# Kernel optimization log

Measured on AMD Instinct MI355X. Metric: run time of the kernel, lower is better.

## Reference

```python
import jax, jax.numpy as jnp
import numpy as np

D_MODEL = 2048
NUM_Q_HEADS = 32
NUM_KV_HEADS = 8
HEAD_DIM = D_MODEL // NUM_Q_HEADS  # 64
NUM_GROUPS = NUM_Q_HEADS // NUM_KV_HEADS  # 4


def setup_inputs() -> dict:
    key = jax.random.key(0)
    ks = jax.random.split(key, 9)
    s = 1.0 / np.sqrt(D_MODEL)
    x = jax.random.normal(ks[0], (2, 2048, D_MODEL), dtype=jnp.float32)
    Wq = jax.random.uniform(ks[1], (D_MODEL, NUM_Q_HEADS * HEAD_DIM), jnp.float32, -s, s)
    bq = jax.random.uniform(ks[2], (NUM_Q_HEADS * HEAD_DIM,), jnp.float32, -s, s)
    Wk = jax.random.uniform(ks[3], (D_MODEL, NUM_KV_HEADS * HEAD_DIM), jnp.float32, -s, s)
    bk = jax.random.uniform(ks[4], (NUM_KV_HEADS * HEAD_DIM,), jnp.float32, -s, s)
    Wv = jax.random.uniform(ks[5], (D_MODEL, NUM_KV_HEADS * HEAD_DIM), jnp.float32, -s, s)
    bv = jax.random.uniform(ks[6], (NUM_KV_HEADS * HEAD_DIM,), jnp.float32, -s, s)
    Wo = jax.random.uniform(ks[7], (D_MODEL, D_MODEL), jnp.float32, -s, s)
    bo = jax.random.uniform(ks[8], (D_MODEL,), jnp.float32, -s, s)
    return {"x": x, "Wq": Wq, "bq": bq, "Wk": Wk, "bk": bk,
            "Wv": Wv, "bv": bv, "Wo": Wo, "bo": bo}


def reference(x, Wq, bq, Wk, bk, Wv, bv, Wo, bo):
    B, T, C = x.shape
    Hkv, G, Dh = NUM_KV_HEADS, NUM_GROUPS, HEAD_DIM
    # projections
    q = (x @ Wq + bq).reshape(B, T, Hkv, G, Dh)   # group G query heads per kv head
    k = (x @ Wk + bk).reshape(B, T, Hkv, Dh)
    v = (x @ Wv + bv).reshape(B, T, Hkv, Dh)
    scale = 1.0 / np.sqrt(Dh).astype(np.float32)
    # scores: [B, Hkv, G, T, T] (kv head broadcast over its G query heads)
    scores = jnp.einsum('btkgd,bskd->bkgts', q, k) * scale
    attn = jax.nn.softmax(scores, axis=-1)
    out = jnp.einsum('bkgts,bskd->btkgd', attn, v).reshape(B, T, C)
    return out @ Wo + bo
```

## Files before the change

### kernel.cpp

```cpp
#include <hip/hip_runtime.h>
#include <cstdint>
#include <cstddef>
#include <math.h>

typedef uint16_t bf16;
typedef __attribute__((ext_vector_type(8))) __bf16 bf16x8;
typedef __attribute__((ext_vector_type(2))) float f32x2;
typedef __attribute__((ext_vector_type(4))) float f32x4;
typedef __attribute__((ext_vector_type(16))) float f32x16;

#define MFMA16(a,b,c) __builtin_amdgcn_mfma_f32_16x16x32_bf16((a),(b),(c),0,0,0)
#define MFMA32(a,b,c) __builtin_amdgcn_mfma_f32_32x32x16_bf16((a),(b),(c),0,0,0)

__device__ __forceinline__ uint16_t f2bf(float f){
  uint32_t u = __float_as_uint(f);
  return (uint16_t)((u + 0x7fffu + ((u >> 16) & 1u)) >> 16);
}
__device__ __forceinline__ uint32_t pk2(float lo, float hi){
  return (uint32_t)f2bf(lo) | ((uint32_t)f2bf(hi) << 16);
}

__device__ __forceinline__ void gload_lds16(const void* g, void* l){
  __builtin_amdgcn_global_load_lds((const __attribute__((address_space(1))) void*)g,
                                   (__attribute__((address_space(3))) void*)l, 16, 0, 0);
}

__global__ void k_convert(const float* __restrict__ in, bf16* __restrict__ out, int n){
  int i = (blockIdx.x * 256 + threadIdx.x) * 4;
  if (i >= n) return;
  float4 v = *reinterpret_cast<const float4*>(in + i);
  uint32_t lo = pk2(v.x, v.y);
  uint32_t hi = pk2(v.z, v.w);
  uint2 pkv = make_uint2(lo, hi);
  *reinterpret_cast<uint2*>(out + i) = pkv;
}

__global__ void k_transposeW(const float* __restrict__ in, bf16* __restrict__ out, int R, int C){
  __shared__ float tile[64][65];
  int c0 = blockIdx.x * 64, r0 = blockIdx.y * 64;
  int t = threadIdx.x;
  int fx = t & 15, fy = t >> 4;
  #pragma unroll
  for (int i = 0; i < 4; i++){
    int r = fy + i*16;
    float4 v = *reinterpret_cast<const float4*>(in + (size_t)(r0 + r)*C + c0 + fx*4);
    tile[r][fx*4+0] = v.x; tile[r][fx*4+1] = v.y;
    tile[r][fx*4+2] = v.z; tile[r][fx*4+3] = v.w;
  }
  __syncthreads();
  int gx = t & 7, gy = t >> 3;
  #pragma unroll
  for (int i = 0; i < 2; i++){
    int c = gy + i*32;
    int rr = gx*8;
    union { bf16 h[8]; uint4 u; } pk_;
    #pragma unroll
    for (int j = 0; j < 8; j++) pk_.h[j] = f2bf(tile[rr+j][c]);
    *reinterpret_cast<uint4*>(out + (size_t)(c0 + c)*R + r0 + rr) = pk_.u;
  }
}

__device__ __forceinline__ void gemm128_core(
    const bf16* __restrict__ Abase, const bf16* __restrict__ Btbase,
    int lda, int ldb, int K, bf16* As, bf16* Bs, f32x4 acc[4][4])
{
  const int tid = threadIdx.x;
  const int wid = tid >> 6, lane = tid & 63;
  const int wr = wid >> 1, wc = wid & 1;
  const int lr = lane & 15, lg = lane >> 4;
  const f32x4 vzero = {0.f, 0.f, 0.f, 0.f};

  #pragma unroll
  for (int m = 0; m < 4; m++)
    #pragma unroll
    for (int n = 0; n < 4; n++)
      acc[m][n] = vzero;

  int srcA[4], srcB[4], dOff[4];
  #pragma unroll
  for (int i = 0; i < 4; i++){
    int d = i*4096 + wid*1024 + lane*16;
    int row = d >> 7, sp = (d >> 4) & 7;
    int sl = sp ^ (row & 7);
    srcA[i] = row * lda + sl * 8;
    srcB[i] = row * ldb + sl * 8;
    dOff[i] = i*4096 + wid*1024;
  }

  for (int k0 = 0; k0 < K; k0 += 64){
    #pragma unroll
    for (int i = 0; i < 4; i++)
      gload_lds16(Abase + k0 + srcA[i], (char*)As + dOff[i]);
    #pragma unroll
    for (int i = 0; i < 4; i++)
      gload_lds16(Btbase + k0 + srcB[i], (char*)Bs + dOff[i]);
    __syncthreads();
    #pragma unroll
    for (int ks = 0; ks < 2; ks++){
      bf16x8 af[4], bfr[4];
      #pragma unroll
      for (int m = 0; m < 4; m++){
        int row = wr*64 + m*16 + lr;
        int sp = (ks*4 + lg) ^ (row & 7);
        af[m] = *reinterpret_cast<const bf16x8*>(As + row*64 + sp*8);
      }
      #pragma unroll
      for (int n = 0; n < 4; n++){
        int row = wc*64 + n*16 + lr;
        int sp = (ks*4 + lg) ^ (row & 7);
        bfr[n] = *reinterpret_cast<const bf16x8*>(Bs + row*64 + sp*8);
      }
      #pragma unroll
      for (int m = 0; m < 4; m++)
        #pragma unroll
        for (int n = 0; n < 4; n++)
          acc[m][n] = MFMA16(af[m], bfr[n], acc[m][n]);
    }
    __syncthreads();
  }
}

__device__ __forceinline__ void gemm256_core(
    const bf16* __restrict__ Abase, const bf16* __restrict__ Btbase,
    char* lds, f32x4 acc[8][4])
{
  const int tid = threadIdx.x;
  const int wid = tid >> 6, lane = tid & 63;
  const int wm = wid >> 2, wn = wid & 3;
  const int lr = lane & 15, lg = lane >> 4;
  const f32x4 vzero = {0.f, 0.f, 0.f, 0.f};
  #pragma unroll
  for (int m = 0; m < 8; m++)
    #pragma unroll
    for (int n = 0; n < 4; n++)
      acc[m][n] = vzero;

  int srcH[2];
  #pragma unroll
  for (int i = 0; i < 2; i++){
    int db = i*8192 + tid*16;
    int row = db >> 7, sp = (db >> 4) & 7, sl = sp ^ (row & 7);
    srcH[i] = row*2048 + sl*8;
  }
  const int dOf = wid*1024;

  int ksl[2];
  #pragma unroll
  for (int ks = 0; ks < 2; ks++) ksl[ks] = (((ks*4 + lg) ^ (lr & 7)) << 4);
  const int aB = wm*16384 + lr*128;
  const int bB = 32768 + (wn >> 1)*16384 + (wn & 1)*8192 + lr*128;

  const bf16* Ab1 = Abase + 128*2048;
  const bf16* Bb1 = Btbase + 128*2048;

  #define STG_HALF(dstOff, gsrc) do { \
    gload_lds16((gsrc) + srcH[0], lds + (dstOff) + dOf); \
    gload_lds16((gsrc) + srcH[1], lds + (dstOff) + 8192 + dOf); \
  } while(0)

  STG_HALF(0,     Abase);
  STG_HALF(16384, Ab1);
  STG_HALF(32768, Btbase);
  STG_HALF(49152, Bb1);
  STG_HALF(65536, Abase + 64);
  asm volatile("s_waitcnt vmcnt(2)" ::: "memory");
  __builtin_amdgcn_s_barrier();

  bf16x8 afr[4][2], bfr[4][2];
  for (int t = 0; t < 32; t++){
    const int bo = (t & 1) * 65536;
    const int nb = bo ^ 65536;

    #pragma unroll
    for (int am = 0; am < 4; am++)
      #pragma unroll
      for (int ks = 0; ks < 2; ks++)
        afr[am][ks] = *reinterpret_cast<const bf16x8*>(lds + bo + aB + am*2048 + ksl[ks]);
    #pragma unroll
    for (int bn = 0; bn < 2; bn++)
      #pragma unroll
      for (int ks = 0; ks < 2; ks++)
        bfr[bn][ks] = *reinterpret_cast<const bf16x8*>(lds + bo + bB + bn*2048 + ksl[ks]);
    if (t < 31) STG_HALF(nb + 16384, Ab1 + (t+1)*64);
    __builtin_amdgcn_s_barrier();
    asm volatile("s_waitcnt lgkmcnt(0)" ::: "memory");
    __builtin_amdgcn_sched_barrier(0);
    __builtin_amdgcn_s_setprio(1);
    #pragma unroll
    for (int am = 0; am < 4; am++)
      #pragma unroll
      for (int bn = 0; bn < 2; bn++)
        #pragma unroll
        for (int ks = 0; ks < 2; ks++)
          acc[am][bn] = MFMA16(afr[am][ks], bfr[bn][ks], acc[am][bn]);
    __builtin_amdgcn_s_setprio(0);
    __builtin_amdgcn_s_barrier();

    #pragma unroll
    for (int bn = 2; bn < 4; bn++)
      #pragma unroll
      for (int ks = 0; ks < 2; ks++)
        bfr[bn][ks] = *reinterpret_cast<const bf16x8*>(lds + bo + bB + bn*2048 + ksl[ks]);
    if (t < 31) STG_HALF(nb + 32768, Btbase + (t+1)*64);
    __builtin_amdgcn_s_barrier();
    asm volatile("s_waitcnt lgkmcnt(0)" ::: "memory");
    __builtin_amdgcn_sched_barrier(0);
    __builtin_amdgcn_s_setprio(1);
    #pragma unroll
    for (int am = 0; am < 4; am++)
      #pragma unroll
      for (int bn = 2; bn < 4; bn++)
        #pragma unroll
        for (int ks = 0; ks < 2; ks++)
          acc[am][bn] = MFMA16(afr[am][ks], bfr[bn][ks], acc[am][bn]);
    __builtin_amdgcn_s_setprio(0);
    __builtin_amdgcn_s_barrier();

    #pragma unroll
    for (int am = 0; am < 4; am++)
      #pragma unroll
      for (int ks = 0; ks < 2; ks++)
        afr[am][ks] = *reinterpret_cast<const bf16x8*>(lds + bo + aB + (am+4)*2048 + ksl[ks]);
    if (t < 31) STG_HALF(nb + 49152, Bb1 + (t+1)*64);
    __builtin_amdgcn_s_barrier();
    asm volatile("s_waitcnt lgkmcnt(0)" ::: "memory");
    __builtin_amdgcn_sched_barrier(0);
    __builtin_amdgcn_s_setprio(1);
    #pragma unroll
    for (int am = 0; am < 4; am++)
      #pragma unroll
      for (int bn = 0; bn < 2; bn++)
        #pragma unroll
        for (int ks = 0; ks < 2; ks++)
          acc[am+4][bn] = MFMA16(afr[am][ks], bfr[bn][ks], acc[am+4][bn]);
    __builtin_amdgcn_s_setprio(0);
    __builtin_amdgcn_s_barrier();

    if (t < 30) STG_HALF(bo, Abase + (t+2)*64);
    __builtin_amdgcn_s_barrier();
    __builtin_amdgcn_s_setprio(1);
    #pragma unroll
    for (int am = 0; am < 4; am++)
      #pragma unroll
      for (int bn = 2; bn < 4; bn++)
        #pragma unroll
        for (int ks = 0; ks < 2; ks++)
          acc[am+4][bn] = MFMA16(afr[am][ks], bfr[bn][ks], acc[am+4][bn]);
    __builtin_amdgcn_s_setprio(0);
    if (t < 30)      asm volatile("s_waitcnt vmcnt(2)" ::: "memory");
    else if (t == 30) asm volatile("s_waitcnt vmcnt(0)" ::: "memory");
    __builtin_amdgcn_sched_barrier(0);
    __builtin_amdgcn_s_barrier();
  }
  #undef STG_HALF
}

__global__ __launch_bounds__(512, 1) void k_qkv(
    const bf16* __restrict__ xb,
    const bf16* __restrict__ WqT, const bf16* __restrict__ WkT, const bf16* __restrict__ WvT,
    const float* __restrict__ bq, const float* __restrict__ bk, const float* __restrict__ bv,
    bf16* __restrict__ qo, bf16* __restrict__ ko, bf16* __restrict__ vtp)
{
  __shared__ __align__(16) char lds[131072];
  int by = blockIdx.y;
  const bf16* Bt; const float* bias; int mode; int y; float scale = 1.f;
  if (by < 8){       y = by;    Bt = WqT + (size_t)y*256*2048; bias = bq + y*256; mode = 0; scale = 0.18033688011112042f; }
  else if (by < 10){ y = by-8;  Bt = WkT + (size_t)y*256*2048; bias = bk + y*256; mode = 1; }
  else {             y = by-10; Bt = WvT + (size_t)y*256*2048; bias = bv + y*256; mode = 2; }
  int m0 = blockIdx.x * 256;
  f32x4 acc[8][4];
  gemm256_core(xb + (size_t)m0*2048, Bt, lds, acc);
  const int tid = threadIdx.x, wid = tid >> 6, lane = tid & 63;
  const int wm = wid >> 2, wn = wid & 3, lr = lane & 15, lg = lane >> 4;
  if (mode == 2){
    #pragma unroll
    for (int bn = 0; bn < 4; bn++){
      int c = wn*64 + bn*16 + lr;
      float bb = bias[c];
      int CL = y*256 + c;
      #pragma unroll
      for (int am = 0; am < 8; am++){
        int row0 = m0 + wm*128 + am*16 + lg*4;
        int bi = row0 >> 11, tl = row0 & 2047;
        union { bf16 h[4]; uint2 u; } pk_;
        #pragma unroll
        for (int r = 0; r < 4; r++) pk_.h[r] = f2bf(acc[am][bn][r] + bb);
        *reinterpret_cast<uint2*>(vtp + ((size_t)bi*512 + CL)*2048 + tl) = pk_.u;
      }
    }
  } else {
    bf16* outp = (mode == 0) ? (qo + y*256) : (ko + y*256);
    int ldc = (mode == 0) ? 2048 : 512;
    #pragma unroll
    for (int bn = 0; bn < 4; bn++){
      int c = wn*64 + bn*16 + lr;
      float bb = bias[c];
      #pragma unroll
      for (int am = 0; am < 8; am++)
        #pragma unroll
        for (int r = 0; r < 4; r++){
          int row = m0 + wm*128 + am*16 + lg*4 + r;
          outp[(size_t)row*ldc + c] = f2bf((acc[am][bn][r] + bb) * scale);
        }
    }
  }
}

__global__ __launch_bounds__(256, 2) void k_oproj(
    const bf16* __restrict__ ab, const bf16* __restrict__ WoT,
    const float* __restrict__ bo, float* __restrict__ outp)
{
  __shared__ __align__(16) bf16 As[128*64];
  __shared__ __align__(16) bf16 Bs[128*64];
  int m0 = blockIdx.x * 128, n0 = blockIdx.y * 128;
  f32x4 acc[4][4];
  gemm128_core(ab + (size_t)m0*2048, WoT + (size_t)n0*2048, 2048, 2048, 2048, As, Bs, acc);
  const int tid = threadIdx.x, wid = tid >> 6, lane = tid & 63;
  const int wr = wid >> 1, wc = wid & 1, lr = lane & 15, lg = lane >> 4;
  #pragma unroll
  for (int n = 0; n < 4; n++){
    int col = n0 + wc*64 + n*16 + lr;
    float bb = bo[col];
    #pragma unroll
    for (int m = 0; m < 4; m++)
      #pragma unroll
      for (int r = 0; r < 4; r++){
        int row = m0 + wr*64 + m*16 + lg*4 + r;
        outp[(size_t)row*2048 + col] = acc[m][n][r] + bb;
      }
  }
}

__global__ __launch_bounds__(512, 2) void k_flash(
    const bf16* __restrict__ q, const bf16* __restrict__ kmat,
    const bf16* __restrict__ vt, bf16* __restrict__ ao)
{
  __shared__ __align__(16) char lds[98304];
  const int tid = threadIdx.x;
  const int wid = tid >> 6, lane = tid & 63;
  const int l31 = lane & 31, hi = lane >> 5;
  const int bh = blockIdx.y;
  const int b = bh >> 5, hq = bh & 31, kvh = hq >> 2;
  const int qt = blockIdx.x;
  const int qrow0 = b*2048 + qt*512 + wid*64;

  bf16x8 qf[2][4];
  #pragma unroll
  for (int g = 0; g < 2; g++){
    const bf16* qrow = q + (size_t)(qrow0 + g*32 + l31)*2048 + hq*64 + hi*8;
    #pragma unroll
    for (int t = 0; t < 4; t++)
      qf[g][t] = *reinterpret_cast<const bf16x8*>(qrow + t*16);
  }

  f32x16 oacc[2][2];
  #pragma unroll
  for (int g = 0; g < 2; g++)
    #pragma unroll
    for (int n = 0; n < 2; n++)
      #pragma unroll
      for (int r = 0; r < 16; r++) oacc[g][n][r] = 0.f;
  float rsg[2][2];
  rsg[0][0]=0.f; rsg[0][1]=0.f; rsg[1][0]=0.f; rsg[1][1]=0.f;
  const f32x16 zv = {0.f,0.f,0.f,0.f,0.f,0.f,0.f,0.f,0.f,0.f,0.f,0.f,0.f,0.f,0.f,0.f};

  const int r7 = l31 & 7;
  int A[4];
  #pragma unroll
  for (int j = 0; j < 4; j++)
    A[j] = l31*128 + (((2*j + hi) ^ r7) << 4);

  const bf16* kbase = kmat + (size_t)b*2048*512 + kvh*64;
  const bf16* vbase = vt + ((size_t)b*512 + kvh*64)*2048;

  int kSrc[2], vSrc[2];
  const int dOf = wid*1024;
  #pragma unroll
  for (int i = 0; i < 2; i++){
    int kdb = i*8192 + tid*16;
    int krow = kdb >> 7, ksp = (kdb >> 4) & 7, ksl = ksp ^ (krow & 7);
    kSrc[i] = krow*512 + ksl*8;
    int o = tid*16;
    int vrow = o >> 7, vsp = (o >> 4) & 7, vsl = vsp ^ (vrow & 7);
    vSrc[i] = vrow*2048 + i*64 + vsl*8;
  }

  #define STAGE(bo, st_) do { \
    const bf16* kb_ = kbase + (size_t)(st_)*128*512; \
    const bf16* vb_ = vbase + (st_)*128; \
    gload_lds16(kb_ + kSrc[0], lds + (bo) + dOf); \
    gload_lds16(kb_ + kSrc[1], lds + (bo) + 8192 + dOf); \
    gload_lds16(vb_ + vSrc[0], lds + 49152 + (bo) + dOf); \
    gload_lds16(vb_ + vSrc[1], lds + 49152 + (bo) + 8192 + dOf); \
  } while(0)

  #define LDK(j, imm) (*reinterpret_cast<const bf16x8*>(lds + kOff + A[j] + (imm)))
  #define LDV(j, imm) (*reinterpret_cast<const bf16x8*>(lds + 49152 + kOff + A[j] + (imm)))

  STAGE(0, 0);
  STAGE(16384, 1);

  int kOff = 0;
  int sOff = 32768;
  for (int st = 0; st < 16; st++){
    if (st == 15) asm volatile("s_waitcnt vmcnt(0)" ::: "memory");
    else          asm volatile("s_waitcnt vmcnt(4)" ::: "memory");
    __builtin_amdgcn_sched_barrier(0);
    __builtin_amdgcn_s_barrier();
    __builtin_amdgcn_sched_barrier(0);
    if (st < 14){
      STAGE(sOff, st+2);
      sOff = (sOff == 32768) ? 0 : sOff + 16384;
    }

    #pragma unroll
    for (int c = 0; c < 2; c++){
      f32x16 sc[2][2];
      __builtin_amdgcn_s_setprio(1);
      #pragma unroll
      for (int t = 0; t < 4; t++){
        bf16x8 af0 = LDK(t, c*8192);
        bf16x8 af1 = LDK(t, c*8192 + 4096);
        if (t == 0){
          sc[0][0] = MFMA32(af0, qf[0][0], zv);
          sc[1][0] = MFMA32(af0, qf[1][0], zv);
          sc[0][1] = MFMA32(af1, qf[0][0], zv);
          sc[1][1] = MFMA32(af1, qf[1][0], zv);
        } else {
          sc[0][0] = MFMA32(af0, qf[0][t], sc[0][0]);
          sc[1][0] = MFMA32(af0, qf[1][t], sc[1][0]);
          sc[0][1] = MFMA32(af1, qf[0][t], sc[0][1]);
          sc[1][1] = MFMA32(af1, qf[1][t], sc[1][1]);
        }
      }
      __builtin_amdgcn_s_setprio(0);

      uint32_t pw[2][2][8];
      #pragma unroll
      for (int g = 0; g < 2; g++){
        #pragma unroll
        for (int n = 0; n < 2; n++)
          #pragma unroll
          for (int j = 0; j < 8; j++){
            float plo = __builtin_amdgcn_exp2f(sc[g][n][2*j]);
            float phi = __builtin_amdgcn_exp2f(sc[g][n][2*j+1]);
            rsg[g][j & 1] += plo + phi;
            asm("v_cvt_pk_bf16_f32 %0, %1, %2" : "=v"(pw[g][n][j]) : "v"(plo), "v"(phi));
          }
        #pragma unroll
        for (int n = 0; n < 2; n++)
          #pragma unroll
          for (int h = 0; h < 2; h++){
            asm volatile("v_permlane32_swap_b32 %0, %1" : "+v"(pw[g][n][h*4+0]), "+v"(pw[g][n][h*4+2]));
            asm volatile("v_permlane32_swap_b32 %0, %1" : "+v"(pw[g][n][h*4+1]), "+v"(pw[g][n][h*4+3]));
          }
      }

      __builtin_amdgcn_s_setprio(1);
      #pragma unroll
      for (int kk = 0; kk < 4; kk++){
        int n = kk >> 1, h = kk & 1;
        union { uint32_t w[4]; bf16x8 v; } pa0, pa1;
        #pragma unroll
        for (int w_ = 0; w_ < 4; w_++){ pa0.w[w_] = pw[0][n][h*4+w_]; pa1.w[w_] = pw[1][n][h*4+w_]; }
        #pragma unroll
        for (int nd = 0; nd < 2; nd++){
          bf16x8 vf = LDV(kk, c*8192 + nd*4096);
          oacc[0][nd] = MFMA32(pa0.v, vf, oacc[0][nd]);
          oacc[1][nd] = MFMA32(pa1.v, vf, oacc[1][nd]);
        }
      }
      __builtin_amdgcn_s_setprio(0);
    }
    kOff = (kOff == 32768) ? 0 : kOff + 16384;
  }
  #undef STAGE
  #undef LDK
  #undef LDV

  #pragma unroll
  for (int g = 0; g < 2; g++){
    float rs = rsg[g][0] + rsg[g][1];
    float l = rs + __shfl_xor(rs, 32);
    float linv = 1.f / l;
    float lv[16];
    #pragma unroll
    for (int r = 0; r < 16; r++){
      int qi = (r & 3) + 8*(r >> 2) + 4*hi;
      lv[r] = __shfl(linv, qi);
    }
    #pragma unroll
    for (int nd = 0; nd < 2; nd++)
      #pragma unroll
      for (int r = 0; r < 16; r++){
        int qi = (r & 3) + 8*(r >> 2) + 4*hi;
        int row = qrow0 + g*32 + qi;
        ao[(size_t)row*2048 + hq*64 + nd*32 + l31] = f2bf(oacc[g][nd][r] * lv[r]);
      }
  }
}

extern "C" void kernel_launch(void* const* d_in, const int* in_sizes, int n_in,
                              void* d_out, int out_size, void* d_ws, size_t ws_size,
                              hipStream_t stream)
{
  const float* x  = (const float*)d_in[0];
  const float* Wq = (const float*)d_in[1];
  const float* bq = (const float*)d_in[2];
  const float* Wk = (const float*)d_in[3];
  const float* bk = (const float*)d_in[4];
  const float* Wv = (const float*)d_in[5];
  const float* bv = (const float*)d_in[6];
  const float* Wo = (const float*)d_in[7];
  const float* bo = (const float*)d_in[8];
  float* out = (float*)d_out;

  char* ws = (char*)d_ws;
  size_t off = 0;
  auto alloc = [&](size_t bytes){ char* p = ws + off; off += (bytes + 255) & ~(size_t)255; return p; };
  bf16* xb  = (bf16*)alloc(2*2048*2048*2);
  bf16* WqT = (bf16*)alloc(2048*2048*2);
  bf16* WkT = (bf16*)alloc(512*2048*2);
  bf16* WvT = (bf16*)alloc(512*2048*2);
  bf16* WoT = (bf16*)alloc(2048*2048*2);
  bf16* qb  = (bf16*)alloc(4096*2048*2);
  bf16* kb  = (bf16*)alloc((size_t)4096*512*2);
  bf16* vtb = (bf16*)alloc((size_t)4096*512*2);
  bf16* aob = xb;

  k_convert<<<8192, 256, 0, stream>>>(x, xb, 2*2048*2048);
  k_transposeW<<<dim3(32,32), 256, 0, stream>>>(Wq, WqT, 2048, 2048);
  k_transposeW<<<dim3(8,32),  256, 0, stream>>>(Wk, WkT, 2048, 512);
  k_transposeW<<<dim3(8,32),  256, 0, stream>>>(Wv, WvT, 2048, 512);
  k_transposeW<<<dim3(32,32), 256, 0, stream>>>(Wo, WoT, 2048, 2048);
  k_qkv<<<dim3(16,12), 512, 0, stream>>>(xb, WqT, WkT, WvT, bq, bk, bv, qb, kb, vtb);
  k_flash<<<dim3(4,64), 512, 0, stream>>>(qb, kb, vtb, aob);
  k_oproj<<<dim3(32,16), 256, 0, stream>>>(aob, WoT, bo, out);
}
```

Before: 194.3 us.

## Replace output projection GEMM with pipelined 256x128 tile kernel

The output projection previously used a simple 128x128 tile GEMM that loaded A and B into LDS, synchronized, computed, and synchronized again, with no overlap. It now uses a 512-thread 256x128 tile core with a triple-buffered A stage and double-buffered B stage. Global-to-LDS loads for later k-steps are issued while MFMAs run, with explicit waitcnt, barrier and priority control. The grid drops from 512 to 256 blocks at one block per CU, which reduces redundant B reads and hides load latency, but risks lower occupancy and tail imbalance.

```diff
diff --git a/kernel.cpp b/kernel.cpp
--- a/kernel.cpp
+++ b/kernel.cpp
@@ -57,66 +57,6 @@
     #pragma unroll
     for (int j = 0; j < 8; j++) pk_.h[j] = f2bf(tile[rr+j][c]);
     *reinterpret_cast<uint4*>(out + (size_t)(c0 + c)*R + r0 + rr) = pk_.u;
-  }
-}
-
-__device__ __forceinline__ void gemm128_core(
-    const bf16* __restrict__ Abase, const bf16* __restrict__ Btbase,
-    int lda, int ldb, int K, bf16* As, bf16* Bs, f32x4 acc[4][4])
-{
-  const int tid = threadIdx.x;
-  const int wid = tid >> 6, lane = tid & 63;
-  const int wr = wid >> 1, wc = wid & 1;
-  const int lr = lane & 15, lg = lane >> 4;
-  const f32x4 vzero = {0.f, 0.f, 0.f, 0.f};
-
-  #pragma unroll
-  for (int m = 0; m < 4; m++)
-    #pragma unroll
-    for (int n = 0; n < 4; n++)
-      acc[m][n] = vzero;
-
-  int srcA[4], srcB[4], dOff[4];
-  #pragma unroll
-  for (int i = 0; i < 4; i++){
-    int d = i*4096 + wid*1024 + lane*16;
-    int row = d >> 7, sp = (d >> 4) & 7;
-    int sl = sp ^ (row & 7);
-    srcA[i] = row * lda + sl * 8;
-    srcB[i] = row * ldb + sl * 8;
-    dOff[i] = i*4096 + wid*1024;
-  }
-
-  for (int k0 = 0; k0 < K; k0 += 64){
-    #pragma unroll
-    for (int i = 0; i < 4; i++)
-      gload_lds16(Abase + k0 + srcA[i], (char*)As + dOff[i]);
-    #pragma unroll
-    for (int i = 0; i < 4; i++)
-      gload_lds16(Btbase + k0 + srcB[i], (char*)Bs + dOff[i]);
-    __syncthreads();
-    #pragma unroll
-    for (int ks = 0; ks < 2; ks++){
-      bf16x8 af[4], bfr[4];
-      #pragma unroll
-      for (int m = 0; m < 4; m++){
-        int row = wr*64 + m*16 + lr;
-        int sp = (ks*4 + lg) ^ (row & 7);
-        af[m] = *reinterpret_cast<const bf16x8*>(As + row*64 + sp*8);
-      }
-      #pragma unroll
-      for (int n = 0; n < 4; n++){
-        int row = wc*64 + n*16 + lr;
-        int sp = (ks*4 + lg) ^ (row & 7);
-        bfr[n] = *reinterpret_cast<const bf16x8*>(Bs + row*64 + sp*8);
-      }
-      #pragma unroll
-      for (int m = 0; m < 4; m++)
-        #pragma unroll
-        for (int n = 0; n < 4; n++)
-          acc[m][n] = MFMA16(af[m], bfr[n], acc[m][n]);
-    }
-    __syncthreads();
   }
 }
 
@@ -253,6 +193,107 @@
     __builtin_amdgcn_s_barrier();
   }
   #undef STG_HALF
+}
+
+__device__ __forceinline__ void gemm256x128_core(
+    const bf16* __restrict__ Abase, const bf16* __restrict__ Btbase,
+    char* lds, f32x4 acc[2][8])
+{
+  const int tid = threadIdx.x;
+  const int wid = tid >> 6, lane = tid & 63;
+  const int lr = lane & 15, lg = lane >> 4;
+  const f32x4 vzero = {0.f, 0.f, 0.f, 0.f};
+  #pragma unroll
+  for (int m = 0; m < 2; m++)
+    #pragma unroll
+    for (int n = 0; n < 8; n++)
+      acc[m][n] = vzero;
+
+  int srcH[2];
+  #pragma unroll
+  for (int i = 0; i < 2; i++){
+    int db = i*8192 + tid*16;
+    int row = db >> 7, sp = (db >> 4) & 7, sl = sp ^ (row & 7);
+    srcH[i] = row*2048 + sl*8;
+  }
+  const int dOf = wid*1024;
+
+  int ksl[2];
+  #pragma unroll
+  for (int ks = 0; ks < 2; ks++) ksl[ks] = (((ks*4 + lg) ^ (lr & 7)) << 4);
+  const int aB = wid*4096 + lr*128;
+  const int bB = lr*128;
+
+  const bf16* Ab1 = Abase + 128*2048;
+
+  #define STG16(dstOff, gsrc) do { \
+    gload_lds16((gsrc) + srcH[0], lds + (dstOff) + dOf); \
+    gload_lds16((gsrc) + srcH[1], lds + (dstOff) + 8192 + dOf); \
+  } while(0)
+  #define STG_A(bufOff, koff) do { \
+    STG16((bufOff),         Abase + (koff)); \
+    STG16((bufOff) + 16384, Ab1  + (koff)); \
+  } while(0)
+
+  STG_A(0, 0);
+  STG16(98304, Btbase);
+  STG_A(32768, 64);
+  asm volatile("s_waitcnt vmcnt(4)" ::: "memory");
+  __builtin_amdgcn_s_barrier();
+
+  int aOff = 0;
+  int aStg = 65536;
+  bf16x8 afr[2], bfr[8];
+  for (int t = 0; t < 32; t++){
+    const int bOff = 98304 + (t & 1) * 16384;
+    const int nbOff = bOff ^ 16384;
+
+    #pragma unroll
+    for (int am = 0; am < 2; am++)
+      afr[am] = *reinterpret_cast<const bf16x8*>(lds + aOff + aB + am*2048 + ksl[0]);
+    #pragma unroll
+    for (int bn = 0; bn < 8; bn++)
+      bfr[bn] = *reinterpret_cast<const bf16x8*>(lds + bOff + bB + bn*2048 + ksl[0]);
+    if (t < 31) STG16(nbOff, Btbase + (t+1)*64);
+    __builtin_amdgcn_s_barrier();
+    asm volatile("s_waitcnt lgkmcnt(0)" ::: "memory");
+    __builtin_amdgcn_sched_barrier(0);
+    __builtin_amdgcn_s_setprio(1);
+    #pragma unroll
+    for (int am = 0; am < 2; am++)
+      #pragma unroll
+      for (int bn = 0; bn < 8; bn++)
+        acc[am][bn] = MFMA16(afr[am], bfr[bn], acc[am][bn]);
+    __builtin_amdgcn_s_setprio(0);
+    __builtin_amdgcn_s_barrier();
+
+    #pragma unroll
+    for (int am = 0; am < 2; am++)
+      afr[am] = *reinterpret_cast<const bf16x8*>(lds + aOff + aB + am*2048 + ksl[1]);
+    #pragma unroll
+    for (int bn = 0; bn < 8; bn++)
+      bfr[bn] = *reinterpret_cast<const bf16x8*>(lds + bOff + bB + bn*2048 + ksl[1]);
+    if (t < 30) STG_A(aStg, (t+2)*64);
+    __builtin_amdgcn_s_barrier();
+    asm volatile("s_waitcnt lgkmcnt(0)" ::: "memory");
+    __builtin_amdgcn_sched_barrier(0);
+    __builtin_amdgcn_s_setprio(1);
+    #pragma unroll
+    for (int am = 0; am < 2; am++)
+      #pragma unroll
+      for (int bn = 0; bn < 8; bn++)
+        acc[am][bn] = MFMA16(afr[am], bfr[bn], acc[am][bn]);
+    __builtin_amdgcn_s_setprio(0);
+    if (t < 30)       asm volatile("s_waitcnt vmcnt(4)" ::: "memory");
+    else if (t == 30) asm volatile("s_waitcnt vmcnt(0)" ::: "memory");
+    __builtin_amdgcn_sched_barrier(0);
+    __builtin_amdgcn_s_barrier();
+
+    aOff = (aOff == 65536) ? 0 : aOff + 32768;
+    aStg = (aStg == 65536) ? 0 : aStg + 32768;
+  }
+  #undef STG16
+  #undef STG_A
 }
 
 __global__ __launch_bounds__(512, 1) void k_qkv(
@@ -306,27 +347,26 @@
   }
 }
 
-__global__ __launch_bounds__(256, 2) void k_oproj(
+__global__ __launch_bounds__(512, 1) void k_oproj(
     const bf16* __restrict__ ab, const bf16* __restrict__ WoT,
     const float* __restrict__ bo, float* __restrict__ outp)
 {
-  __shared__ __align__(16) bf16 As[128*64];
-  __shared__ __align__(16) bf16 Bs[128*64];
-  int m0 = blockIdx.x * 128, n0 = blockIdx.y * 128;
-  f32x4 acc[4][4];
-  gemm128_core(ab + (size_t)m0*2048, WoT + (size_t)n0*2048, 2048, 2048, 2048, As, Bs, acc);
+  __shared__ __align__(16) char lds[131072];
+  int m0 = blockIdx.x * 256, n0 = blockIdx.y * 128;
+  f32x4 acc[2][8];
+  gemm256x128_core(ab + (size_t)m0*2048, WoT + (size_t)n0*2048, lds, acc);
   const int tid = threadIdx.x, wid = tid >> 6, lane = tid & 63;
-  const int wr = wid >> 1, wc = wid & 1, lr = lane & 15, lg = lane >> 4;
-  #pragma unroll
-  for (int n = 0; n < 4; n++){
-    int col = n0 + wc*64 + n*16 + lr;
+  const int lr = lane & 15, lg = lane >> 4;
+  #pragma unroll
+  for (int bn = 0; bn < 8; bn++){
+    int col = n0 + bn*16 + lr;
     float bb = bo[col];
     #pragma unroll
-    for (int m = 0; m < 4; m++)
+    for (int am = 0; am < 2; am++)
       #pragma unroll
       for (int r = 0; r < 4; r++){
-        int row = m0 + wr*64 + m*16 + lg*4 + r;
-        outp[(size_t)row*2048 + col] = acc[m][n][r] + bb;
+        int row = m0 + wid*32 + am*16 + lg*4 + r;
+        outp[(size_t)row*2048 + col] = acc[am][bn][r] + bb;
       }
   }
 }
@@ -535,5 +575,5 @@
   k_transposeW<<<dim3(32,32), 256, 0, stream>>>(Wo, WoT, 2048, 2048);
   k_qkv<<<dim3(16,12), 512, 0, stream>>>(xb, WqT, WkT, WvT, bq, bk, bv, qb, kb, vtb);
   k_flash<<<dim3(4,64), 512, 0, stream>>>(qb, kb, vtb, aob);
-  k_oproj<<<dim3(32,16), 256, 0, stream>>>(aob, WoT, bo, out);
-}
+  k_oproj<<<dim3(16,16), 512, 0, stream>>>(aob, WoT, bo, out);
+}
```

Measured after the change: 194.4 us. About the same (+0.0%).
